# Performance work log

Measured on AMD Instinct MI355X. Metric: run time of the kernel, lower is better.

## Reference

```python
import jax, jax.numpy as jnp
import numpy as np

# PyTorch LSTM cell with zero initial (h, c): W_hh @ h0 == 0, and c = sigmoid(i)*tanh(g)
# since the forget-gate term f*c0 vanishes. Gate order in torch: i, f, g, o.
# b here is the combined b_ih + b_hh (identical math).

def lstm_step0(x, Wih, b):
    pre = x @ Wih.T + b                      # (N, 4H)
    i, f, g, o = jnp.split(pre, 4, axis=-1)
    c = jax.nn.sigmoid(i) * jnp.tanh(g)
    return jax.nn.sigmoid(o) * jnp.tanh(c)   # (N, H)


def setup_inputs() -> dict:
    key = jax.random.key(0)
    ks = jax.random.split(key, 13)
    num_ts, num_periods, F = 128, 256, 128
    GH, NH, NF = 512, 256, 10
    s = lambda k, shape, fan: (jax.random.normal(k, shape, jnp.float32) / np.sqrt(fan))
    return {
        "X": jax.random.normal(ks[0], (num_ts, num_periods, F), jnp.float32),
        "g_Wih0": s(ks[1], (4 * GH, F), F),
        "g_b0": s(ks[2], (4 * GH,), GH),
        "g_Wih1": s(ks[3], (4 * GH, GH), GH),
        "g_b1": s(ks[4], (4 * GH,), GH),
        "aff_W": s(ks[5], (NF, GH), GH),
        "aff_b": s(ks[6], (NF,), GH),
        "n_Wih0": s(ks[7], (4 * NH, F), F),
        "n_b0": s(ks[8], (4 * NH,), NH),
        "n_Wih1": s(ks[9], (4 * NH, NH), NH),
        "n_b1": s(ks[10], (4 * NH,), NH),
        "noise_W": s(ks[11], (1, NH), NH),
        "noise_b": s(ks[12], (1,), NH),
    }


def reference(X, g_Wih0, g_b0, g_Wih1, g_b1, aff_W, aff_b,
              n_Wih0, n_b0, n_Wih1, n_b1, noise_W, noise_b):
    num_ts, num_periods, num_feats = X.shape
    x = X.reshape(-1, num_feats)             # (num_ts*num_periods, F)

    # Global factor branch: 2-layer LSTM single step from zero state
    hg = lstm_step0(lstm_step0(x, g_Wih0, g_b0), g_Wih1, g_b1)
    hg = jax.nn.relu(hg)
    mus = (hg @ aff_W.T + aff_b).sum(axis=-1).reshape(num_ts, num_periods)

    # Noise branch: 2-layer LSTM single step from zero state
    hn = lstm_step0(lstm_step0(x, n_Wih0, n_b0), n_Wih1, n_b1)
    hn = jax.nn.relu(hn)
    sigmas = jax.nn.softplus(hn @ noise_W.T + noise_b)  # log(1+exp(.)), stable
    sigmas = sigmas.reshape(num_ts, num_periods) + 1e-6
    return mus, sigmas
```

## Files before the change

kernel.cpp:

```cpp
#include <hip/hip_runtime.h>
#include <hip/hip_bf16.h>
#include <hip/hip_fp16.h>

typedef _Float16 h8_t __attribute__((ext_vector_type(8)));
typedef _Float16 h4_t __attribute__((ext_vector_type(4)));
typedef float f4_t __attribute__((ext_vector_type(4)));

#define M_ROWS 32768

__device__ __forceinline__ void gload_lds16(const void* g, void* l) {
  __builtin_amdgcn_global_load_lds((const __attribute__((address_space(1))) void*)g,
                                   (__attribute__((address_space(3))) void*)l, 16, 0, 0);
}

__device__ __forceinline__ float sigmoid_f(float x) { return 1.f / (1.f + __expf(-x)); }
__device__ __forceinline__ float tanh_f(float x) { return 1.f - 2.f / (__expf(2.f * x) + 1.f); }

struct GArgs {
  const _Float16* A;
  const _Float16* W;
  const float* bias;
  _Float16* Hout;
  const float* rvec;
  float* partial;
};

__global__ void prep_all(const float* __restrict__ X, const float* __restrict__ gW0,
                         const float* __restrict__ gW1, const float* __restrict__ nW0,
                         const float* __restrict__ nW1, const float* __restrict__ aff_W,
                         const float* __restrict__ aff_b,
                         _Float16* __restrict__ Xh, _Float16* __restrict__ Wg0,
                         _Float16* __restrict__ Wg1, _Float16* __restrict__ Wn0,
                         _Float16* __restrict__ Wn1,
                         float* __restrict__ pg, float* __restrict__ pn,
                         float* __restrict__ wsum) {
  int b = blockIdx.x;
  const float* s; _Float16* d; int base;
  if (b < 4096)      { s = X;   d = Xh;  base = b; }
  else if (b < 4352) { s = gW0; d = Wg0; base = b - 4096; }
  else if (b < 5376) { s = gW1; d = Wg1; base = b - 4352; }
  else if (b < 5504) { s = nW0; d = Wn0; base = b - 5376; }
  else if (b < 5760) { s = nW1; d = Wn1; base = b - 5504; }
  else if (b < 5888) {
    int i = (b - 5760) * 256 + threadIdx.x;
    pg[i] = 0.f; pn[i] = 0.f;
    return;
  } else {
    int j = (b - 5888) * 256 + threadIdx.x;
    float sum = 0.f;
#pragma unroll
    for (int r = 0; r < 10; ++r) sum += aff_W[r * 512 + j];
    wsum[j] = sum;
    if (j == 0) {
      float bs = 0.f;
#pragma unroll
      for (int r = 0; r < 10; ++r) bs += aff_b[r];
      wsum[512] = bs;
    }
    return;
  }
  int i4 = (base * 256 + threadIdx.x) * 4;
  float4 v = *(const float4*)(s + i4);
  h4_t o;
  o[0] = (_Float16)v.x; o[1] = (_Float16)v.y; o[2] = (_Float16)v.z; o[3] = (_Float16)v.w;
  *(h4_t*)(d + i4) = o;
}

template <int K_DIM, int H_DIM, bool FUSE>
__device__ __forceinline__ void gemm_body(const GArgs& ga, int h0, int m0,
                                          _Float16* As, _Float16* Bs) {
  const int tid = threadIdx.x;
  const int wid = tid >> 6;
  const int lane = tid & 63;
  const int wave_m = wid >> 1;
  const int wave_h = wid & 1;
  const int q = lane >> 4;
  const int tcol = lane & 15;

  constexpr int NT = K_DIM / 32;
  constexpr int A_BYTES = 64 * 32 * 2;
  constexpr int B_BYTES = 4 * 64 * 32 * 2;
  constexpr int A_ELEMS = 64 * 32;
  constexpr int B_ELEMS = 4 * 64 * 32;

  const _Float16* aptr; int aoff;
  {
    int o = (wid << 10) + (lane << 4);
    int row = o >> 6;
    int cl = (o >> 4) & 3;
    int cg = cl ^ ((row >> 1) & 3);
    aptr = ga.A + (size_t)(m0 + row) * K_DIM + cg * 8;
    aoff = o;
  }
  const _Float16* bptr[4]; int boff[4];
#pragma unroll
  for (int c = 0; c < 4; ++c) {
    int o = ((wid * 4 + c) << 10) + (lane << 4);
    int pan = o >> 12;
    int row = (o >> 6) & 63;
    int cl = (o >> 4) & 3;
    int cg = cl ^ ((row >> 1) & 3);
    bptr[c] = ga.W + (size_t)(pan * H_DIM + h0 + row) * K_DIM + cg * 8;
    boff[c] = o;
  }
  int a_rd[2];
#pragma unroll
  for (int mi = 0; mi < 2; ++mi) {
    int r = wave_m * 32 + mi * 16 + tcol;
    a_rd[mi] = r * 32 + (q ^ ((r >> 1) & 3)) * 8;
  }
  int b_rd[2];
#pragma unroll
  for (int ni = 0; ni < 2; ++ni) {
    int j = wave_h * 32 + ni * 16 + tcol;
    b_rd[ni] = j * 32 + (q ^ ((j >> 1) & 3)) * 8;
  }

  f4_t acc[3][2][2];
#pragma unroll
  for (int p = 0; p < 3; ++p)
#pragma unroll
    for (int mi = 0; mi < 2; ++mi)
#pragma unroll
      for (int ni = 0; ni < 2; ++ni) acc[p][mi][ni] = (f4_t){0.f, 0.f, 0.f, 0.f};

  gload_lds16(aptr, (char*)As + aoff);
#pragma unroll
  for (int c = 0; c < 4; ++c) gload_lds16(bptr[c], (char*)Bs + boff[c]);
  aptr += 32;
#pragma unroll
  for (int c = 0; c < 4; ++c) bptr[c] += 32;

#pragma unroll
  for (int kk = 0; kk < NT; ++kk) {
    const int cur = kk & 1;
    const int nxt = cur ^ 1;
    if (kk < NT - 1) {
      gload_lds16(aptr, (char*)As + nxt * A_BYTES + aoff);
#pragma unroll
      for (int c = 0; c < 4; ++c) gload_lds16(bptr[c], (char*)Bs + nxt * B_BYTES + boff[c]);
      aptr += 32;
#pragma unroll
      for (int c = 0; c < 4; ++c) bptr[c] += 32;
      asm volatile("s_waitcnt vmcnt(5)" ::: "memory");
    } else {
      asm volatile("s_waitcnt vmcnt(0)" ::: "memory");
    }
    __builtin_amdgcn_s_barrier();
    asm volatile("" ::: "memory");

    h8_t af[2];
#pragma unroll
    for (int mi = 0; mi < 2; ++mi) af[mi] = *(const h8_t*)&As[cur * A_ELEMS + a_rd[mi]];
#pragma unroll
    for (int p = 0; p < 3; ++p) {
      const int pb = (p == 0 ? 0 : (p == 1 ? 2 : 3)) * 2048;
#pragma unroll
      for (int ni = 0; ni < 2; ++ni) {
        h8_t bf = *(const h8_t*)&Bs[cur * B_ELEMS + pb + b_rd[ni]];
#pragma unroll
        for (int mi = 0; mi < 2; ++mi)
          acc[p][mi][ni] = __builtin_amdgcn_mfma_f32_16x16x32_f16(af[mi], bf, acc[p][mi][ni], 0, 0, 0);
      }
    }
    asm volatile("" ::: "memory");
    if (kk < NT - 1) __builtin_amdgcn_s_barrier();
  }

  const int mrow0 = m0 + wave_m * 32;
  const int jcol0 = h0 + wave_h * 32;

  if constexpr (!FUSE) {
#pragma unroll
    for (int ni = 0; ni < 2; ++ni) {
      int j = jcol0 + ni * 16 + tcol;
      float bi = ga.bias[j];
      float bg = ga.bias[2 * H_DIM + j];
      float bo = ga.bias[3 * H_DIM + j];
#pragma unroll
      for (int mi = 0; mi < 2; ++mi)
#pragma unroll
        for (int r = 0; r < 4; ++r) {
          float pi = acc[0][mi][ni][r] + bi;
          float pgt = acc[1][mi][ni][r] + bg;
          float po = acc[2][mi][ni][r] + bo;
          float cc = sigmoid_f(pi) * tanh_f(pgt);
          float hh = sigmoid_f(po) * tanh_f(cc);
          int m = mrow0 + mi * 16 + q * 4 + r;
          ga.Hout[(size_t)m * H_DIM + j] = (_Float16)hh;
        }
    }
  } else {
    float rsum[2][4];
#pragma unroll
    for (int mi = 0; mi < 2; ++mi)
#pragma unroll
      for (int r = 0; r < 4; ++r) rsum[mi][r] = 0.f;
#pragma unroll
    for (int ni = 0; ni < 2; ++ni) {
      int j = jcol0 + ni * 16 + tcol;
      float bi = ga.bias[j];
      float bg = ga.bias[2 * H_DIM + j];
      float bo = ga.bias[3 * H_DIM + j];
      float rv = ga.rvec[j];
#pragma unroll
      for (int mi = 0; mi < 2; ++mi)
#pragma unroll
        for (int r = 0; r < 4; ++r) {
          float pi = acc[0][mi][ni][r] + bi;
          float pgt = acc[1][mi][ni][r] + bg;
          float po = acc[2][mi][ni][r] + bo;
          float cc = sigmoid_f(pi) * tanh_f(pgt);
          float hh = sigmoid_f(po) * tanh_f(cc);
          hh = fmaxf(hh, 0.f);
          rsum[mi][r] += hh * rv;
        }
    }
#pragma unroll
    for (int mi = 0; mi < 2; ++mi)
#pragma unroll
      for (int r = 0; r < 4; ++r) {
        float v = rsum[mi][r];
        v += __shfl_xor(v, 1);
        v += __shfl_xor(v, 2);
        v += __shfl_xor(v, 4);
        v += __shfl_xor(v, 8);
        if (tcol == 0) atomicAdd(&ga.partial[mrow0 + mi * 16 + q * 4 + r], v);
      }
  }
}

__device__ __forceinline__ void swizzle_xy(int& x, int& y) {
  int lin = blockIdx.y * gridDim.x + blockIdx.x;
  int c = lin & 7;
  int r = lin >> 3;
  y = r % 12;
  x = c * 64 + r / 12;
}

__global__ __launch_bounds__(256, 4) void layer1_fused(GArgs g, GArgs n) {
  __shared__ __align__(16) _Float16 As[2 * 64 * 32];
  __shared__ __align__(16) _Float16 Bs[2 * 4 * 64 * 32];
  int x, y; swizzle_xy(x, y);
  if (y < 8) gemm_body<128, 512, false>(g, y * 64, x * 64, As, Bs);
  else       gemm_body<128, 256, false>(n, (y - 8) * 64, x * 64, As, Bs);
}

__global__ __launch_bounds__(256, 4) void layer2_fused(GArgs g, GArgs n) {
  __shared__ __align__(16) _Float16 As[2 * 64 * 32];
  __shared__ __align__(16) _Float16 Bs[2 * 4 * 64 * 32];
  int x, y; swizzle_xy(x, y);
  if (y < 8) gemm_body<512, 512, true>(g, y * 64, x * 64, As, Bs);
  else       gemm_body<256, 256, true>(n, (y - 8) * 64, x * 64, As, Bs);
}

__global__ void finalize(const float* __restrict__ pg, const float* __restrict__ pn,
                         const float* __restrict__ wsum, const float* __restrict__ noise_b,
                         float* __restrict__ out) {
  int i = blockIdx.x * blockDim.x + threadIdx.x;
  out[i] = pg[i] + wsum[512];
  float x = pn[i] + noise_b[0];
  float sp = fmaxf(x, 0.f) + log1pf(expf(-fabsf(x)));
  out[M_ROWS + i] = sp + 1e-6f;
}

extern "C" void kernel_launch(void* const* d_in, const int* in_sizes, int n_in,
                              void* d_out, int out_size, void* d_ws, size_t ws_size,
                              hipStream_t stream) {
  const float* X       = (const float*)d_in[0];
  const float* g_Wih0  = (const float*)d_in[1];
  const float* g_b0    = (const float*)d_in[2];
  const float* g_Wih1  = (const float*)d_in[3];
  const float* g_b1    = (const float*)d_in[4];
  const float* aff_W   = (const float*)d_in[5];
  const float* aff_b   = (const float*)d_in[6];
  const float* n_Wih0  = (const float*)d_in[7];
  const float* n_b0    = (const float*)d_in[8];
  const float* n_Wih1  = (const float*)d_in[9];
  const float* n_b1    = (const float*)d_in[10];
  const float* noise_W = (const float*)d_in[11];
  const float* noise_b = (const float*)d_in[12];
  float* out = (float*)d_out;

  char* w = (char*)d_ws;
  _Float16* Xh  = (_Float16*)w; w += (size_t)M_ROWS * 128 * 2;
  _Float16* Wg0 = (_Float16*)w; w += 2048 * 128 * 2;
  _Float16* Wg1 = (_Float16*)w; w += 2048 * 512 * 2;
  _Float16* Wn0 = (_Float16*)w; w += 1024 * 128 * 2;
  _Float16* Wn1 = (_Float16*)w; w += 1024 * 256 * 2;
  _Float16* h1g = (_Float16*)w; w += (size_t)M_ROWS * 512 * 2;
  _Float16* h1n = (_Float16*)w; w += (size_t)M_ROWS * 256 * 2;
  float* pg   = (float*)w; w += (size_t)M_ROWS * 4;
  float* pn   = (float*)w; w += (size_t)M_ROWS * 4;
  float* wsum = (float*)w; w += 4096;

  prep_all<<<5890, 256, 0, stream>>>(X, g_Wih0, g_Wih1, n_Wih0, n_Wih1, aff_W, aff_b,
                                     Xh, Wg0, Wg1, Wn0, Wn1, pg, pn, wsum);

  GArgs l1g = {Xh, Wg0, g_b0, h1g, nullptr, nullptr};
  GArgs l1n = {Xh, Wn0, n_b0, h1n, nullptr, nullptr};
  layer1_fused<<<dim3(M_ROWS / 64, 12), 256, 0, stream>>>(l1g, l1n);

  GArgs l2g = {h1g, Wg1, g_b1, nullptr, wsum, pg};
  GArgs l2n = {h1n, Wn1, n_b1, nullptr, noise_W, pn};
  layer2_fused<<<dim3(M_ROWS / 64, 12), 256, 0, stream>>>(l2g, l2n);

  finalize<<<M_ROWS / 256, 256, 0, stream>>>(pg, pn, wsum, noise_b, out);
}
```

Measured before the change: 291.4 us.

## Read weights directly from global and enlarge M tile to 128 rows

B (weight) fragments are now loaded straight from global memory into registers instead of being staged through LDS, and only the activation tile goes through LDS. The block grows to 512 threads covering 128 rows with a 64-wide K step and a new 8-way XOR swizzle. The aim is to cut LDS traffic and barriers per MFMA and to reuse each weight tile across more rows. The cost is that weight loads become uncoalesced per-lane 16-byte global reads that depend on L2 hits and may stall MFMAs, since no prefetch pipeline covers them.

New measurement: 467.3 us. 1.6x slower.

```diff
diff --git a/kernel.cpp b/kernel.cpp
--- a/kernel.cpp
+++ b/kernel.cpp
@@ -67,8 +67,8 @@
 }
 
 template <int K_DIM, int H_DIM, bool FUSE>
-__device__ __forceinline__ void gemm_body(const GArgs& ga, int h0, int m0,
-                                          _Float16* As, _Float16* Bs) {
+__device__ __forceinline__ void gemm_body(const GArgs& ga, int h0, int m_base,
+                                          _Float16* As) {
   const int tid = threadIdx.x;
   const int wid = tid >> 6;
   const int lane = tid & 63;
@@ -77,44 +77,40 @@
   const int q = lane >> 4;
   const int tcol = lane & 15;
 
-  constexpr int NT = K_DIM / 32;
-  constexpr int A_BYTES = 64 * 32 * 2;
-  constexpr int B_BYTES = 4 * 64 * 32 * 2;
-  constexpr int A_ELEMS = 64 * 32;
-  constexpr int B_ELEMS = 4 * 64 * 32;
-
-  const _Float16* aptr; int aoff;
-  {
-    int o = (wid << 10) + (lane << 4);
-    int row = o >> 6;
-    int cl = (o >> 4) & 3;
-    int cg = cl ^ ((row >> 1) & 3);
-    aptr = ga.A + (size_t)(m0 + row) * K_DIM + cg * 8;
-    aoff = o;
-  }
-  const _Float16* bptr[4]; int boff[4];
-#pragma unroll
-  for (int c = 0; c < 4; ++c) {
-    int o = ((wid * 4 + c) << 10) + (lane << 4);
-    int pan = o >> 12;
-    int row = (o >> 6) & 63;
-    int cl = (o >> 4) & 3;
-    int cg = cl ^ ((row >> 1) & 3);
-    bptr[c] = ga.W + (size_t)(pan * H_DIM + h0 + row) * K_DIM + cg * 8;
-    boff[c] = o;
-  }
-  int a_rd[2];
-#pragma unroll
-  for (int mi = 0; mi < 2; ++mi) {
-    int r = wave_m * 32 + mi * 16 + tcol;
-    a_rd[mi] = r * 32 + (q ^ ((r >> 1) & 3)) * 8;
-  }
-  int b_rd[2];
-#pragma unroll
-  for (int ni = 0; ni < 2; ++ni) {
-    int j = wave_h * 32 + ni * 16 + tcol;
-    b_rd[ni] = j * 32 + (q ^ ((j >> 1) & 3)) * 8;
-  }
+  constexpr int NT = K_DIM / 64;
+  constexpr int A_BYTES = 128 * 64 * 2;
+  constexpr int A_ELEMS = 128 * 64;
+
+  const _Float16* aptr[2]; int aoff[2];
+#pragma unroll
+  for (int c = 0; c < 2; ++c) {
+    int o = ((wid * 2 + c) << 10) + (lane << 4);
+    int row = o >> 7, pch = (o >> 4) & 7;
+    int lch = pch ^ (row & 7);
+    aptr[c] = ga.A + (size_t)(m_base + row) * K_DIM + lch * 8;
+    aoff[c] = o;
+  }
+  const _Float16* bp[3][2];
+#pragma unroll
+  for (int p = 0; p < 3; ++p) {
+    const int gb = (p == 0 ? 0 : (p == 1 ? 2 * H_DIM : 3 * H_DIM));
+#pragma unroll
+    for (int ni = 0; ni < 2; ++ni) {
+      int j = h0 + wave_h * 32 + ni * 16 + tcol;
+      bp[p][ni] = ga.W + (size_t)(gb + j) * K_DIM + q * 8;
+    }
+  }
+  int a_rd[2][2];
+#pragma unroll
+  for (int ks = 0; ks < 2; ++ks)
+#pragma unroll
+    for (int mi = 0; mi < 2; ++mi) {
+      int r = wave_m * 32 + mi * 16 + tcol;
+      int c = ks * 4 + q;
+      a_rd[ks][mi] = r * 64 + (c ^ (r & 7)) * 8;
+    }
+
+  const int jcol0 = h0 + wave_h * 32;
 
   f4_t acc[3][2][2];
 #pragma unroll
@@ -124,52 +120,48 @@
 #pragma unroll
       for (int ni = 0; ni < 2; ++ni) acc[p][mi][ni] = (f4_t){0.f, 0.f, 0.f, 0.f};
 
-  gload_lds16(aptr, (char*)As + aoff);
-#pragma unroll
-  for (int c = 0; c < 4; ++c) gload_lds16(bptr[c], (char*)Bs + boff[c]);
-  aptr += 32;
-#pragma unroll
-  for (int c = 0; c < 4; ++c) bptr[c] += 32;
-
-#pragma unroll
-  for (int kk = 0; kk < NT; ++kk) {
-    const int cur = kk & 1;
+#pragma unroll
+  for (int c = 0; c < 2; ++c) gload_lds16(aptr[c], (char*)As + aoff[c]);
+#pragma unroll
+  for (int c = 0; c < 2; ++c) aptr[c] += 64;
+
+#pragma unroll
+  for (int s = 0; s < NT; ++s) {
+    const int cur = s & 1;
     const int nxt = cur ^ 1;
-    if (kk < NT - 1) {
-      gload_lds16(aptr, (char*)As + nxt * A_BYTES + aoff);
-#pragma unroll
-      for (int c = 0; c < 4; ++c) gload_lds16(bptr[c], (char*)Bs + nxt * B_BYTES + boff[c]);
-      aptr += 32;
-#pragma unroll
-      for (int c = 0; c < 4; ++c) bptr[c] += 32;
-      asm volatile("s_waitcnt vmcnt(5)" ::: "memory");
+    if (s < NT - 1) {
+#pragma unroll
+      for (int c = 0; c < 2; ++c) gload_lds16(aptr[c], (char*)As + nxt * A_BYTES + aoff[c]);
+#pragma unroll
+      for (int c = 0; c < 2; ++c) aptr[c] += 64;
+      asm volatile("s_waitcnt vmcnt(2)" ::: "memory");
     } else {
       asm volatile("s_waitcnt vmcnt(0)" ::: "memory");
     }
     __builtin_amdgcn_s_barrier();
     asm volatile("" ::: "memory");
 
-    h8_t af[2];
-#pragma unroll
-    for (int mi = 0; mi < 2; ++mi) af[mi] = *(const h8_t*)&As[cur * A_ELEMS + a_rd[mi]];
-#pragma unroll
-    for (int p = 0; p < 3; ++p) {
-      const int pb = (p == 0 ? 0 : (p == 1 ? 2 : 3)) * 2048;
-#pragma unroll
-      for (int ni = 0; ni < 2; ++ni) {
-        h8_t bf = *(const h8_t*)&Bs[cur * B_ELEMS + pb + b_rd[ni]];
-#pragma unroll
-        for (int mi = 0; mi < 2; ++mi)
-          acc[p][mi][ni] = __builtin_amdgcn_mfma_f32_16x16x32_f16(af[mi], bf, acc[p][mi][ni], 0, 0, 0);
+#pragma unroll
+    for (int ks = 0; ks < 2; ++ks) {
+      h8_t af[2];
+#pragma unroll
+      for (int mi = 0; mi < 2; ++mi) af[mi] = *(const h8_t*)&As[cur * A_ELEMS + a_rd[ks][mi]];
+#pragma unroll
+      for (int p = 0; p < 3; ++p) {
+#pragma unroll
+        for (int ni = 0; ni < 2; ++ni) {
+          h8_t bf = *(const h8_t*)(bp[p][ni] + s * 64 + ks * 32);
+#pragma unroll
+          for (int mi = 0; mi < 2; ++mi)
+            acc[p][mi][ni] = __builtin_amdgcn_mfma_f32_16x16x32_f16(af[mi], bf, acc[p][mi][ni], 0, 0, 0);
+        }
       }
     }
     asm volatile("" ::: "memory");
-    if (kk < NT - 1) __builtin_amdgcn_s_barrier();
-  }
-
-  const int mrow0 = m0 + wave_m * 32;
-  const int jcol0 = h0 + wave_h * 32;
-
+    if (s < NT - 1) __builtin_amdgcn_s_barrier();
+  }
+
+  const int mrow0 = m_base + wave_m * 32;
   if constexpr (!FUSE) {
 #pragma unroll
     for (int ni = 0; ni < 2; ++ni) {
@@ -234,24 +226,23 @@
   int lin = blockIdx.y * gridDim.x + blockIdx.x;
   int c = lin & 7;
   int r = lin >> 3;
+  int xpx = gridDim.x >> 3;
   y = r % 12;
-  x = c * 64 + r / 12;
-}
-
-__global__ __launch_bounds__(256, 4) void layer1_fused(GArgs g, GArgs n) {
-  __shared__ __align__(16) _Float16 As[2 * 64 * 32];
-  __shared__ __align__(16) _Float16 Bs[2 * 4 * 64 * 32];
+  x = c * xpx + r / 12;
+}
+
+__global__ __launch_bounds__(512, 4) void layer1_fused(GArgs g, GArgs n) {
+  __shared__ __align__(16) _Float16 As[2 * 128 * 64];
   int x, y; swizzle_xy(x, y);
-  if (y < 8) gemm_body<128, 512, false>(g, y * 64, x * 64, As, Bs);
-  else       gemm_body<128, 256, false>(n, (y - 8) * 64, x * 64, As, Bs);
-}
-
-__global__ __launch_bounds__(256, 4) void layer2_fused(GArgs g, GArgs n) {
-  __shared__ __align__(16) _Float16 As[2 * 64 * 32];
-  __shared__ __align__(16) _Float16 Bs[2 * 4 * 64 * 32];
+  if (y < 8) gemm_body<128, 512, false>(g, y * 64, x * 128, As);
+  else       gemm_body<128, 256, false>(n, (y - 8) * 64, x * 128, As);
+}
+
+__global__ __launch_bounds__(512, 4) void layer2_fused(GArgs g, GArgs n) {
+  __shared__ __align__(16) _Float16 As[2 * 128 * 64];
   int x, y; swizzle_xy(x, y);
-  if (y < 8) gemm_body<512, 512, true>(g, y * 64, x * 64, As, Bs);
-  else       gemm_body<256, 256, true>(n, (y - 8) * 64, x * 64, As, Bs);
+  if (y < 8) gemm_body<512, 512, true>(g, y * 64, x * 128, As);
+  else       gemm_body<256, 256, true>(n, (y - 8) * 64, x * 128, As);
 }
 
 __global__ void finalize(const float* __restrict__ pg, const float* __restrict__ pn,
@@ -299,11 +290,11 @@
 
   GArgs l1g = {Xh, Wg0, g_b0, h1g, nullptr, nullptr};
   GArgs l1n = {Xh, Wn0, n_b0, h1n, nullptr, nullptr};
-  layer1_fused<<<dim3(M_ROWS / 64, 12), 256, 0, stream>>>(l1g, l1n);
+  layer1_fused<<<dim3(256, 12), 512, 0, stream>>>(l1g, l1n);
 
   GArgs l2g = {h1g, Wg1, g_b1, nullptr, wsum, pg};
   GArgs l2n = {h1n, Wn1, n_b1, nullptr, noise_W, pn};
-  layer2_fused<<<dim3(M_ROWS / 64, 12), 256, 0, stream>>>(l2g, l2n);
+  layer2_fused<<<dim3(256, 12), 512, 0, stream>>>(l2g, l2n);
 
   finalize<<<M_ROWS / 256, 256, 0, stream>>>(pg, pn, wsum, noise_b, out);
 }
```
